# Optimization experiments

Hardware: AMD Instinct MI355X
Metric: run time of the kernel (lower is better)

Reference implementation:

```python
import jax, jax.numpy as jnp
import numpy as np

B, S, IN_DIM, HID = 8, 2048, 1024, 1024


def setup_inputs() -> dict:
    key = jax.random.key(0)
    k1, k2, k3, k4, k5 = jax.random.split(key, 5)
    vec = jax.random.normal(k1, (B, S, IN_DIM), dtype=jnp.float32)
    # nn.Linear-style init scale
    wq_w = jax.random.normal(k2, (HID, IN_DIM), dtype=jnp.float32) / np.sqrt(IN_DIM)
    wq_b = jax.random.normal(k3, (HID,), dtype=jnp.float32) * 0.02
    lin_w = jax.random.normal(k4, (1, HID), dtype=jnp.float32) / np.sqrt(HID)
    lin_b = jax.random.normal(k5, (1,), dtype=jnp.float32) * 0.02
    return {"vec": vec, "wq_w": wq_w, "wq_b": wq_b, "lin_w": lin_w, "lin_b": lin_b}


def reference(vec, wq_w, wq_b, lin_w, lin_b):
    # NOTE: the original forward applies self.wq to BOTH q and k (wk/nq/nk unused).
    q = jnp.einsum('bsi,hi->bsh', vec, wq_w) + wq_b          # [B,S,H]
    ret = jnp.einsum('bsx,bsy->bxy', q, q)                    # [B,H,H] bilinear
    ret = jax.nn.relu(ret)
    out = jnp.einsum('bxy,y->bx', ret, lin_w[0]) + lin_b[0]   # Linear(H,1) -> [B,H]
    return out
```

## Files before the change

### kernel.cpp

```cpp
#include <hip/hip_runtime.h>


#define BM 128
#define BN 128

typedef short     bf16x8 __attribute__((ext_vector_type(8)));
typedef unsigned short u16x8 __attribute__((ext_vector_type(8)));
typedef float     f32x4 __attribute__((ext_vector_type(4)));

__device__ inline unsigned short f2bf(float f) {
  unsigned int u = __float_as_uint(f);
  u += 0x7fffu + ((u >> 16) & 1u);
  return (unsigned short)(u >> 16);
}

__device__ inline u16x8 pack8(float4 a, float4 b) {
  u16x8 r;
  r[0] = f2bf(a.x); r[1] = f2bf(a.y); r[2] = f2bf(a.z); r[3] = f2bf(a.w);
  r[4] = f2bf(b.x); r[5] = f2bf(b.y); r[6] = f2bf(b.z); r[7] = f2bf(b.w);
  return r;
}

__device__ inline void async16(unsigned short* lds, const unsigned short* g) {
  __builtin_amdgcn_global_load_lds(
      (const __attribute__((address_space(1))) void*)g,
      (__attribute__((address_space(3))) void*)lds,
      16, 0, 0);
}

__global__ void init_out(float* __restrict__ out, const float* __restrict__ lin_b) {
  int i = blockIdx.x * 256 + threadIdx.x;
  if (i < 8192) out[i] = lin_b[0];
}

__global__ __launch_bounds__(256) void cvt_bf16(
    const float* __restrict__ src, unsigned short* __restrict__ dst, int n8)
{
  int i = blockIdx.x * 256 + threadIdx.x;
  if (i < n8) {
    const float4* s = (const float4*)(src + (size_t)i * 8);
    float4 a = s[0], b = s[1];
    *(u16x8*)(dst + (size_t)i * 8) = pack8(a, b);
  }
}

__global__ __launch_bounds__(256) void gemm_q(
    const unsigned short* __restrict__ A, const unsigned short* __restrict__ Bm,
    const float* __restrict__ bias, unsigned short* __restrict__ qT)
{
  __shared__ unsigned short As[BM * 32];
  __shared__ unsigned short Bs[BN * 32];

  const int m0 = blockIdx.y * BM;
  const int n0 = blockIdx.x * BN;
  const int t    = threadIdx.x;
  const int lane = t & 63;
  const int wave = t >> 6;
  const int wm = (wave >> 1) * 64;
  const int wn = (wave & 1) * 64;
  const int quad = lane >> 4;
  const int lrow = lane & 15;

  const int srow = t >> 2;
  const int gcol = (((t & 3) ^ ((srow >> 1) & 3)) << 3);
  const unsigned short* gA0 = A  + (size_t)(m0 + srow) * 1024 + gcol;
  const unsigned short* gA1 = gA0 + (size_t)64 * 1024;
  const unsigned short* gB0 = Bm + (size_t)(n0 + srow) * 1024 + gcol;
  const unsigned short* gB1 = gB0 + (size_t)64 * 1024;

  const int rc = (quad ^ ((lrow >> 1) & 3)) << 3;

  f32x4 acc[4][4];
#pragma unroll
  for (int i = 0; i < 4; ++i)
#pragma unroll
    for (int j = 0; j < 4; ++j) acc[i][j] = (f32x4){0.f, 0.f, 0.f, 0.f};

  for (int k0 = 0; k0 < 1024; k0 += 32) {
    async16(&As[t * 8],        gA0 + k0);
    async16(&As[2048 + t * 8], gA1 + k0);
    async16(&Bs[t * 8],        gB0 + k0);
    async16(&Bs[2048 + t * 8], gB1 + k0);
    __syncthreads();

    bf16x8 af[4], bfr[4];
#pragma unroll
    for (int i = 0; i < 4; ++i)
      af[i] = *(const bf16x8*)&As[(wm + i * 16 + lrow) * 32 + rc];
#pragma unroll
    for (int j = 0; j < 4; ++j)
      bfr[j] = *(const bf16x8*)&Bs[(wn + j * 16 + lrow) * 32 + rc];
#pragma unroll
    for (int i = 0; i < 4; ++i)
#pragma unroll
      for (int j = 0; j < 4; ++j)
        acc[i][j] = __builtin_amdgcn_mfma_f32_16x16x32_bf16(af[i], bfr[j], acc[i][j], 0, 0, 0);
    __syncthreads();
  }

#pragma unroll
  for (int i = 0; i < 4; ++i) {
    const int mb = m0 + wm + i * 16 + quad * 4;
#pragma unroll
    for (int r = 0; r < 4; ++r) {
      const float bv = bias[mb + r];
#pragma unroll
      for (int j = 0; j < 4; ++j) {
        const int n = n0 + wn + j * 16 + lrow;
        qT[(size_t)(mb + r) * 16384 + n] = f2bf(acc[i][j][r] + bv);
      }
    }
  }
}

__global__ __launch_bounds__(256) void gemm_q_fused(
    const float* __restrict__ Wq, const float* __restrict__ V,
    const float* __restrict__ bias, unsigned short* __restrict__ qT)
{
  __shared__ unsigned short As[BM * 32];
  __shared__ unsigned short Bs[BN * 32];

  const int m0 = blockIdx.y * BM;
  const int n0 = blockIdx.x * BN;
  const int t    = threadIdx.x;
  const int lane = t & 63;
  const int wave = t >> 6;
  const int wm = (wave >> 1) * 64;
  const int wn = (wave & 1) * 64;
  const int quad = lane >> 4;
  const int lrow = lane & 15;

  const int sr = t >> 1;
  const int sc = (t & 1) << 4;
  const float* gA = Wq + (size_t)(m0 + sr) * 1024 + sc;
  const float* gB = V  + (size_t)(n0 + sr) * 1024 + sc;

  f32x4 acc[4][4];
#pragma unroll
  for (int i = 0; i < 4; ++i)
#pragma unroll
    for (int j = 0; j < 4; ++j) acc[i][j] = (f32x4){0.f, 0.f, 0.f, 0.f};

  for (int k0 = 0; k0 < 1024; k0 += 32) {
    const float4* a4 = (const float4*)(gA + k0);
    const float4* b4 = (const float4*)(gB + k0);
    float4 av0 = a4[0], av1 = a4[1], av2 = a4[2], av3 = a4[3];
    float4 bv0 = b4[0], bv1 = b4[1], bv2 = b4[2], bv3 = b4[3];
    *(u16x8*)&As[sr * 32 + sc]     = pack8(av0, av1);
    *(u16x8*)&As[sr * 32 + sc + 8] = pack8(av2, av3);
    *(u16x8*)&Bs[sr * 32 + sc]     = pack8(bv0, bv1);
    *(u16x8*)&Bs[sr * 32 + sc + 8] = pack8(bv2, bv3);
    __syncthreads();

    bf16x8 af[4], bfr[4];
#pragma unroll
    for (int i = 0; i < 4; ++i)
      af[i] = *(const bf16x8*)&As[(wm + i * 16 + lrow) * 32 + quad * 8];
#pragma unroll
    for (int j = 0; j < 4; ++j)
      bfr[j] = *(const bf16x8*)&Bs[(wn + j * 16 + lrow) * 32 + quad * 8];
#pragma unroll
    for (int i = 0; i < 4; ++i)
#pragma unroll
      for (int j = 0; j < 4; ++j)
        acc[i][j] = __builtin_amdgcn_mfma_f32_16x16x32_bf16(af[i], bfr[j], acc[i][j], 0, 0, 0);
    __syncthreads();
  }

#pragma unroll
  for (int i = 0; i < 4; ++i) {
    const int mb = m0 + wm + i * 16 + quad * 4;
#pragma unroll
    for (int r = 0; r < 4; ++r) {
      const float bv = bias[mb + r];
#pragma unroll
      for (int j = 0; j < 4; ++j) {
        const int n = n0 + wn + j * 16 + lrow;
        qT[(size_t)(mb + r) * 16384 + n] = f2bf(acc[i][j][r] + bv);
      }
    }
  }
}

__global__ __launch_bounds__(256) void syrk_dot(
    const unsigned short* __restrict__ qT, const float* __restrict__ W,
    float* __restrict__ out)
{
  __shared__ unsigned short As[BM * 64];
  __shared__ unsigned short Bs[BN * 64];

  const int bb = blockIdx.z;
  const int x0 = blockIdx.y * BM;
  const int y0 = blockIdx.x * BN;
  const int t    = threadIdx.x;
  const int lane = t & 63;
  const int wave = t >> 6;
  const int wm = (wave >> 1) * 64;
  const int wn = (wave & 1) * 64;
  const int quad = lane >> 4;
  const int lrow = lane & 15;

  const int srow = t >> 3;
  const int gcol = (((t & 7) ^ (srow & 7)) << 3);
  const size_t cbase = (size_t)bb * 2048 + gcol;
  const unsigned short* gA = qT + (size_t)(x0 + srow) * 16384 + cbase;
  const unsigned short* gB = qT + (size_t)(y0 + srow) * 16384 + cbase;

  f32x4 acc[4][4];
#pragma unroll
  for (int i = 0; i < 4; ++i)
#pragma unroll
    for (int j = 0; j < 4; ++j) acc[i][j] = (f32x4){0.f, 0.f, 0.f, 0.f};

  for (int k0 = 0; k0 < 2048; k0 += 64) {
#pragma unroll
    for (int p = 0; p < 4; ++p) {
      async16(&As[p * 2048 + t * 8], gA + (size_t)p * 32 * 16384 + k0);
      async16(&Bs[p * 2048 + t * 8], gB + (size_t)p * 32 * 16384 + k0);
    }
    __syncthreads();

#pragma unroll
    for (int kk = 0; kk < 2; ++kk) {
      const int rc = (((kk * 4 + quad) ^ (lrow & 7)) << 3);
      bf16x8 af[4], bfr[4];
#pragma unroll
      for (int i = 0; i < 4; ++i)
        af[i] = *(const bf16x8*)&As[(wm + i * 16 + lrow) * 64 + rc];
#pragma unroll
      for (int j = 0; j < 4; ++j)
        bfr[j] = *(const bf16x8*)&Bs[(wn + j * 16 + lrow) * 64 + rc];
#pragma unroll
      for (int i = 0; i < 4; ++i)
#pragma unroll
        for (int j = 0; j < 4; ++j)
          acc[i][j] = __builtin_amdgcn_mfma_f32_16x16x32_bf16(af[i], bfr[j], acc[i][j], 0, 0, 0);
    }
    __syncthreads();
  }

  float wv[4];
#pragma unroll
  for (int j = 0; j < 4; ++j) wv[j] = W[y0 + wn + j * 16 + lrow];

#pragma unroll
  for (int i = 0; i < 4; ++i) {
#pragma unroll
    for (int r = 0; r < 4; ++r) {
      float p = 0.f;
#pragma unroll
      for (int j = 0; j < 4; ++j) {
        float v = acc[i][j][r];
        v = v > 0.f ? v : 0.f;
        p += v * wv[j];
      }
#pragma unroll
      for (int off = 1; off < 16; off <<= 1) p += __shfl_xor(p, off, 64);
      if (lrow == 0) {
        const int x = x0 + wm + i * 16 + quad * 4 + r;
        atomicAdd(&out[bb * 1024 + x], p);
      }
    }
  }
}

extern "C" void kernel_launch(void* const* d_in, const int* in_sizes, int n_in,
                              void* d_out, int out_size, void* d_ws, size_t ws_size,
                              hipStream_t stream) {
  const float* vec   = (const float*)d_in[0];
  const float* wq_w  = (const float*)d_in[1];
  const float* wq_b  = (const float*)d_in[2];
  const float* lin_w = (const float*)d_in[3];
  const float* lin_b = (const float*)d_in[4];
  float* out = (float*)d_out;

  unsigned short* qT = (unsigned short*)d_ws;
  const size_t need = (size_t)(32 + 32 + 2) * 1024 * 1024;

  init_out<<<dim3(32), dim3(256), 0, stream>>>(out, lin_b);

  if (ws_size >= need) {
    unsigned short* vecbf = qT + (size_t)16 * 1024 * 1024;
    unsigned short* wqbf  = vecbf + (size_t)16 * 1024 * 1024;
    cvt_bf16<<<dim3(8192), dim3(256), 0, stream>>>(vec,  vecbf, 16777216 / 8);
    cvt_bf16<<<dim3(512),  dim3(256), 0, stream>>>(wq_w, wqbf,  1048576 / 8);
    gemm_q<<<dim3(128, 8), dim3(256), 0, stream>>>(wqbf, vecbf, wq_b, qT);
  } else {
    gemm_q_fused<<<dim3(128, 8), dim3(256), 0, stream>>>(wq_w, vec, wq_b, qT);
  }
  syrk_dot<<<dim3(8, 8, 8), dim3(256), 0, stream>>>(qT, lin_w, out);
}
```

Measured before the change: 192.2 us.

## Exploit Gram matrix symmetry in syrk_dot and fuse prep kernels

The bilinear q^T q is symmetric, so syrk_dot now computes only the 36 lower-triangular 128x128 tiles per batch instead of 64. Each off-diagonal tile adds its transposed contribution with an extra column reduction weighted by lin_w. Separately, the two bf16 conversion kernels and the output init are merged into one prep launch to cut launch count. The price is extra atomics and reduction work in off-diagonal tiles, plus a small triangular-index loop per block.

```diff
diff --git a/kernel.cpp b/kernel.cpp
--- a/kernel.cpp
+++ b/kernel.cpp
@@ -28,20 +28,28 @@
       16, 0, 0);
 }
 
+__global__ __launch_bounds__(256) void prep(
+    const float* __restrict__ vec, unsigned short* __restrict__ vecbf,
+    const float* __restrict__ wq,  unsigned short* __restrict__ wqbf,
+    const float* __restrict__ lin_b, float* __restrict__ out)
+{
+  const int gid = blockIdx.x * 256 + threadIdx.x;
+  if (blockIdx.x < 8192) {
+    const float4* s = (const float4*)(vec + (size_t)gid * 8);
+    float4 a = s[0], b = s[1];
+    *(u16x8*)(vecbf + (size_t)gid * 8) = pack8(a, b);
+    if (gid < 8192) out[gid] = lin_b[0];
+  } else {
+    const int i = gid - 8192 * 256;
+    const float4* s = (const float4*)(wq + (size_t)i * 8);
+    float4 a = s[0], b = s[1];
+    *(u16x8*)(wqbf + (size_t)i * 8) = pack8(a, b);
+  }
+}
+
 __global__ void init_out(float* __restrict__ out, const float* __restrict__ lin_b) {
   int i = blockIdx.x * 256 + threadIdx.x;
   if (i < 8192) out[i] = lin_b[0];
-}
-
-__global__ __launch_bounds__(256) void cvt_bf16(
-    const float* __restrict__ src, unsigned short* __restrict__ dst, int n8)
-{
-  int i = blockIdx.x * 256 + threadIdx.x;
-  if (i < n8) {
-    const float4* s = (const float4*)(src + (size_t)i * 8);
-    float4 a = s[0], b = s[1];
-    *(u16x8*)(dst + (size_t)i * 8) = pack8(a, b);
-  }
 }
 
 __global__ __launch_bounds__(256) void gemm_q(
@@ -190,8 +198,14 @@
   __shared__ unsigned short Bs[BN * 64];
 
   const int bb = blockIdx.z;
-  const int x0 = blockIdx.y * BM;
-  const int y0 = blockIdx.x * BN;
+  const int job = blockIdx.x;
+  int tx = 0;
+  while ((tx + 1) * (tx + 2) / 2 <= job) ++tx;
+  const int ty = job - tx * (tx + 1) / 2;
+  const int x0 = tx * BM;
+  const int y0 = ty * BN;
+  const bool diag = (tx == ty);
+
   const int t    = threadIdx.x;
   const int lane = t & 63;
   const int wave = t >> 6;
@@ -239,6 +253,8 @@
     __syncthreads();
   }
 
+  float* ob = out + bb * 1024;
+
   float wv[4];
 #pragma unroll
   for (int j = 0; j < 4; ++j) wv[j] = W[y0 + wn + j * 16 + lrow];
@@ -256,10 +272,34 @@
       }
 #pragma unroll
       for (int off = 1; off < 16; off <<= 1) p += __shfl_xor(p, off, 64);
-      if (lrow == 0) {
-        const int x = x0 + wm + i * 16 + quad * 4 + r;
-        atomicAdd(&out[bb * 1024 + x], p);
-      }
+      if (lrow == 0)
+        atomicAdd(&ob[x0 + wm + i * 16 + quad * 4 + r], p);
+    }
+  }
+
+  if (!diag) {
+    float wx[4][4];
+#pragma unroll
+    for (int i = 0; i < 4; ++i)
+#pragma unroll
+      for (int r = 0; r < 4; ++r)
+        wx[i][r] = W[x0 + wm + i * 16 + quad * 4 + r];
+
+#pragma unroll
+    for (int j = 0; j < 4; ++j) {
+      float pc = 0.f;
+#pragma unroll
+      for (int i = 0; i < 4; ++i)
+#pragma unroll
+        for (int r = 0; r < 4; ++r) {
+          float v = acc[i][j][r];
+          v = v > 0.f ? v : 0.f;
+          pc += v * wx[i][r];
+        }
+      pc += __shfl_xor(pc, 16, 64);
+      pc += __shfl_xor(pc, 32, 64);
+      if (quad == 0)
+        atomicAdd(&ob[y0 + wn + j * 16 + lrow], pc);
     }
   }
 }
@@ -277,16 +317,14 @@
   unsigned short* qT = (unsigned short*)d_ws;
   const size_t need = (size_t)(32 + 32 + 2) * 1024 * 1024;
 
-  init_out<<<dim3(32), dim3(256), 0, stream>>>(out, lin_b);
-
   if (ws_size >= need) {
     unsigned short* vecbf = qT + (size_t)16 * 1024 * 1024;
     unsigned short* wqbf  = vecbf + (size_t)16 * 1024 * 1024;
-    cvt_bf16<<<dim3(8192), dim3(256), 0, stream>>>(vec,  vecbf, 16777216 / 8);
-    cvt_bf16<<<dim3(512),  dim3(256), 0, stream>>>(wq_w, wqbf,  1048576 / 8);
+    prep<<<dim3(8192 + 512), dim3(256), 0, stream>>>(vec, vecbf, wq_w, wqbf, lin_b, out);
     gemm_q<<<dim3(128, 8), dim3(256), 0, stream>>>(wqbf, vecbf, wq_b, qT);
   } else {
+    init_out<<<dim3(32), dim3(256), 0, stream>>>(out, lin_b);
     gemm_q_fused<<<dim3(128, 8), dim3(256), 0, stream>>>(wq_w, vec, wq_b, qT);
   }
-  syrk_dot<<<dim3(8, 8, 8), dim3(256), 0, stream>>>(qT, lin_w, out);
-}
+  syrk_dot<<<dim3(36, 1, 8), dim3(256), 0, stream>>>(qT, lin_w, out);
+}
```

Result: faster. 186.6 us (-2.9%).
